# Optimization experiments

Measured on AMD Instinct MI355X. Metric: run time of the kernel, lower is better.

Reference implementation:

```python
import jax, jax.numpy as jnp
import numpy as np
import math

B, S, D, H = 2, 2048, 1024, 16
DK = D // H  # 64
THETA = 500000.0


def setup_inputs() -> dict:
    key = jax.random.key(0)
    ks = jax.random.split(key, 6)
    x = jax.random.normal(ks[0], (B, S, D), dtype=jnp.float32)
    # RoPE frequencies: inv_freq = theta^{-(2i/dk)}, angles = pos * inv_freq
    inv_freq = 1.0 / (THETA ** (jnp.arange(0, DK, 2, dtype=jnp.float32) / DK))  # [DK/2]
    angles = jnp.arange(S, dtype=jnp.float32)[:, None] * inv_freq[None, :]      # [S, DK/2]
    freqs_cos = jnp.cos(angles)
    freqs_sin = jnp.sin(angles)
    # causal additive mask [B, S, S]: 0 on/below diagonal, -1e9 above
    causal = jnp.tril(jnp.ones((S, S), dtype=bool))
    mask = jnp.where(causal, 0.0, -1e9).astype(jnp.float32)
    mask = jnp.broadcast_to(mask, (B, S, S))
    scale = 0.02
    wq = jax.random.normal(ks[1], (D, D), dtype=jnp.float32) * scale
    wk = jax.random.normal(ks[2], (D, D), dtype=jnp.float32) * scale
    wv = jax.random.normal(ks[3], (D, D), dtype=jnp.float32) * scale
    wo = jax.random.normal(ks[4], (D, D), dtype=jnp.float32) * scale
    return {"x": x, "freqs_cos": freqs_cos, "freqs_sin": freqs_sin,
            "mask": mask, "wq": wq, "wk": wk, "wv": wv, "wo": wo}


def _apply_rope(t, cos, sin):
    # t: [B, S, H, DK]; cos/sin: [S, DK/2]
    tr = t.reshape(*t.shape[:-1], DK // 2, 2)
    t0, t1 = tr[..., 0], tr[..., 1]
    c = cos[None, :, None, :]
    s = sin[None, :, None, :]
    out = jnp.stack([t0 * c - t1 * s, t0 * s + t1 * c], axis=-1)
    return out.reshape(*t.shape)


def reference(x, freqs_cos, freqs_sin, mask, wq, wk, wv, wo):
    b, s, d = x.shape
    # nn.Linear(bias=False): y = x @ W^T, W is [out, in]
    q = jnp.einsum('bsd,ed->bse', x, wq).reshape(b, s, H, DK)
    k = jnp.einsum('bsd,ed->bse', x, wk).reshape(b, s, H, DK)
    v = jnp.einsum('bsd,ed->bse', x, wv).reshape(b, s, H, DK)
    q = _apply_rope(q, freqs_cos, freqs_sin)
    k = _apply_rope(k, freqs_cos, freqs_sin)
    inv_sqrt_dk = 1.0 / math.sqrt(DK)
    # scores: [B, H, S, S]
    scores = jnp.einsum('bqhd,bkhd->bhqk', q, k) * inv_sqrt_dk
    scores = scores + mask[:, None, :, :]
    # NOTE: the original module divides by sqrt(d_k) a SECOND time before softmax
    attn = jax.nn.softmax(scores * inv_sqrt_dk, axis=-1)
    out = jnp.einsum('bhqk,bkhd->bqhd', attn, v).reshape(b, s, d)
    return jnp.einsum('bsd,ed->bse', out, wo)
```

## Files before the change

kernel.cpp:

```cpp
#include <hip/hip_runtime.h>
#include <stdint.h>

#define Bq 2
#define Sq 2048
#define Dq 1024
#define Hq 16
#define DKq 64

typedef unsigned short u16;
typedef __attribute__((ext_vector_type(8))) __bf16 bf8;
typedef __attribute__((ext_vector_type(4))) __bf16 bf4;
typedef __attribute__((ext_vector_type(4))) float fx4;
typedef __attribute__((ext_vector_type(8))) unsigned short us8;
typedef __attribute__((ext_vector_type(4))) unsigned short us4;

__device__ __forceinline__ u16 f2bf(float f) {
    union { float f; unsigned int i; } v; v.f = f;
    unsigned int r = v.i + 0x7FFFu + ((v.i >> 16) & 1u);
    return (u16)(r >> 16);
}

__device__ __forceinline__ void gll16(const void* g, void* l) {
    typedef __attribute__((address_space(1))) void GV;
    typedef __attribute__((address_space(3))) void LV;
    __builtin_amdgcn_global_load_lds((GV*)g, (LV*)l, 16, 0, 0);
}

__global__ void __launch_bounds__(256) cvt_all(const float* __restrict__ x,
                                               const float* __restrict__ wq,
                                               const float* __restrict__ wk,
                                               const float* __restrict__ wv,
                                               const float* __restrict__ wo,
                                               u16* __restrict__ ws) {
    int blk = blockIdx.x;
    const float* s;
    u16* d;
    int i;
    if (blk < 4096)      { s = x;  d = ws;           i = blk * 256 + threadIdx.x; }
    else if (blk < 5120) { s = wq; d = ws + 4194304; i = (blk - 4096) * 256 + threadIdx.x; }
    else if (blk < 6144) { s = wk; d = ws + 5242880; i = (blk - 5120) * 256 + threadIdx.x; }
    else if (blk < 7168) { s = wv; d = ws + 6291456; i = (blk - 6144) * 256 + threadIdx.x; }
    else                 { s = wo; d = ws + 7340032; i = (blk - 7168) * 256 + threadIdx.x; }
    float4 v = *(const float4*)(s + (size_t)i * 4);
    us4 o;
    o[0] = f2bf(v.x); o[1] = f2bf(v.y); o[2] = f2bf(v.z); o[3] = f2bf(v.w);
    *(us4*)(d + (size_t)i * 4) = o;
}

template<int MODE>
__global__ void __launch_bounds__(256) gemm_bt(
    const u16* __restrict__ A,
    const u16* __restrict__ W0, const u16* __restrict__ W1, const u16* __restrict__ W2,
    u16* __restrict__ O0, u16* __restrict__ O1, u16* __restrict__ O2,
    float* __restrict__ Of,
    const float* __restrict__ fc, const float* __restrict__ fs)
{
    constexpr int K = 1024;
    __shared__ __align__(16) u16 As[2][128 * 32];
    __shared__ __align__(16) u16 Bs[2][128 * 32];
    const int tid = threadIdx.x;
    const int lane = tid & 63, wid = tid >> 6;
    const int wr = wid >> 1, wc = wid & 1;
    const int fr = lane & 15, fq = lane >> 4;

    int L = blockIdx.x + 8 * (blockIdx.y + 32 * blockIdx.z);
    int chunk = gridDim.z * 4;
    int X = L & 7, C = L >> 3;
    int bx = C & 7;
    int P = X * chunk + (C >> 3);
    int by = P & 31, bz = P >> 5;
    const int m0 = by * 128, n0 = bx * 128;

    const u16* Wm = W0;
    u16* Ob = O0;
    if (MODE == 1) {
        if (bz == 1)      { Wm = W1; Ob = O1; }
        else if (bz == 2) { Wm = W2; Ob = O2; }
    }

    const int arow = tid >> 2;
    const int acol = (tid & 3) * 8;
    const u16* ga = A  + (size_t)(m0 + arow) * K + acol;
    const u16* gb = Wm + (size_t)(n0 + arow) * K + acol;

    fx4 acc[4][4] = {};

    gll16(ga,          As[0] + tid * 8);
    gll16(ga + 64 * K, As[0] + tid * 8 + 2048);
    gll16(gb,          Bs[0] + tid * 8);
    gll16(gb + 64 * K, Bs[0] + tid * 8 + 2048);
    __syncthreads();
    int cur = 0;

    for (int k0 = 0; k0 < K; k0 += 32) {
        if (k0 + 32 < K) {
            const u16* gan = ga + k0 + 32;
            const u16* gbn = gb + k0 + 32;
            gll16(gan,          As[cur ^ 1] + tid * 8);
            gll16(gan + 64 * K, As[cur ^ 1] + tid * 8 + 2048);
            gll16(gbn,          Bs[cur ^ 1] + tid * 8);
            gll16(gbn + 64 * K, Bs[cur ^ 1] + tid * 8 + 2048);
        }
        bf8 af[4], bfv[4];
        #pragma unroll
        for (int i = 0; i < 4; ++i)
            af[i] = *(const bf8*)(&As[cur][(wr * 64 + i * 16 + fr) * 32 + fq * 8]);
        #pragma unroll
        for (int j = 0; j < 4; ++j)
            bfv[j] = *(const bf8*)(&Bs[cur][(wc * 64 + j * 16 + fr) * 32 + fq * 8]);
        #pragma unroll
        for (int i = 0; i < 4; ++i)
            #pragma unroll
            for (int j = 0; j < 4; ++j)
                acc[i][j] = __builtin_amdgcn_mfma_f32_16x16x32_bf16(af[i], bfv[j], acc[i][j], 0, 0, 0);
        __syncthreads();
        cur ^= 1;
    }

    if (MODE == 0) {
        #pragma unroll
        for (int i = 0; i < 4; ++i)
            #pragma unroll
            for (int j = 0; j < 4; ++j)
                #pragma unroll
                for (int r = 0; r < 4; ++r) {
                    int m = m0 + wr * 64 + i * 16 + fq * 4 + r;
                    int n = n0 + wc * 64 + j * 16 + fr;
                    Of[(size_t)m * 1024 + n] = acc[i][j][r];
                }
    } else if (bz == 2) {
        #pragma unroll
        for (int i = 0; i < 4; ++i)
            #pragma unroll
            for (int j = 0; j < 4; ++j) {
                int n = n0 + wc * 64 + j * 16 + fr;
                int mb = m0 + wr * 64 + i * 16 + fq * 4;
                int b = mb >> 11, s = mb & 2047;
                int h = n >> 6, dk = n & 63;
                bf4 pk;
                #pragma unroll
                for (int r = 0; r < 4; ++r) pk[r] = (__bf16)acc[i][j][r];
                *(bf4*)((__bf16*)Ob + (((size_t)(b * Hq + h)) * DKq + dk) * Sq + s) = pk;
            }
    } else {
        #pragma unroll
        for (int i = 0; i < 4; ++i)
            #pragma unroll
            for (int j = 0; j < 4; ++j) {
                int n = n0 + wc * 64 + j * 16 + fr;
                int h = n >> 6, dk = n & 63;
                int ip = dk >> 1;
                float sgn = (dk & 1) ? 1.f : -1.f;
                #pragma unroll
                for (int r = 0; r < 4; ++r) {
                    int m = m0 + wr * 64 + i * 16 + fq * 4 + r;
                    int b = m >> 11, s = m & 2047;
                    float v = acc[i][j][r];
                    float pv = __shfl_xor(v, 1);
                    float c  = fc[s * 32 + ip];
                    float sn = fs[s * 32 + ip];
                    float o = v * c + sgn * pv * sn;
                    ((__bf16*)Ob)[(((size_t)(b * Hq + h)) * Sq + s) * DKq + dk] = (__bf16)o;
                }
            }
    }
}

__device__ __forceinline__ int swz(int row) { return ((row & 7) ^ ((row >> 3) & 7)) << 4; }

__global__ void __launch_bounds__(512, 4) attn_k(const u16* __restrict__ Q,
                                                 const u16* __restrict__ Kg,
                                                 const u16* __restrict__ Vtg,
                                                 u16* __restrict__ AO) {
    int L = blockIdx.x + 32 * blockIdx.y;
    int X = L & 7, C = L >> 3;
    const int bh = X * 4 + (C & 3);
    const int Qt = 31 - (C >> 2);
    const int b = bh >> 4, h = bh & 15;
    const int tid = threadIdx.x, lane = tid & 63, wid = tid >> 6;
    const int wq4 = wid & 3, par = wid >> 2;
    const int fr = lane & 15, fq = lane >> 4;
    const int swzfr = swz(fr);

    __shared__ __align__(16) u16 Ks[2][64 * 64];
    __shared__ __align__(16) u16 Vs[2][64 * 64];
    __shared__ __align__(16) u16 Ps[8][16 * 64];
    __shared__ float Lx[4][64];

    const u16* Kp = Kg  + (size_t)bh * Sq * 64;
    const u16* Vp = Vtg + (size_t)bh * 64 * Sq;
    const int q0 = Qt * 64;
    const int nt = Qt + 1;
    const int NS = (nt + 1) >> 1;

    bf8 qf0, qf1;
    {
        const u16* Qp = Q + ((size_t)bh * Sq + q0) * 64;
        int qr = wq4 * 16 + fr;
        qf0 = *(const bf8*)(Qp + qr * 64 + fq * 8);
        qf1 = *(const bf8*)(Qp + qr * 64 + fq * 8 + 32);
    }

    fx4 oacc[4] = {};
    float l_loc = 0.f;

    const int srow = tid >> 3;
    const int sce  = (tid & 7) * 8;
    const int ldst = srow * 128 + (((tid & 7) * 16) ^ swz(srow));

    us8 kreg[2], vreg[2];
    #pragma unroll
    for (int c = 0; c < 2; ++c) {
        int t = c < nt ? c : nt - 1;
        kreg[c] = *(const us8*)(Kp + ((size_t)t * 64 + srow) * 64 + sce);
        vreg[c] = *(const us8*)(Vp + (size_t)srow * Sq + t * 64 + sce);
    }
    #pragma unroll
    for (int c = 0; c < 2; ++c) {
        *(us8*)((char*)Ks[c] + ldst) = kreg[c];
        *(us8*)((char*)Vs[c] + ldst) = vreg[c];
    }
    if (NS > 1) {
        #pragma unroll
        for (int c = 0; c < 2; ++c) {
            int t = 2 + c < nt ? 2 + c : nt - 1;
            kreg[c] = *(const us8*)(Kp + ((size_t)t * 64 + srow) * 64 + sce);
            vreg[c] = *(const us8*)(Vp + (size_t)srow * Sq + t * 64 + sce);
        }
    }
    __syncthreads();

    #pragma unroll 1
    for (int sp = 0; sp < NS; ++sp) {
        const int t = 2 * sp + par;
        if (t < nt) {
            const char* Kb = (const char*)Ks[par];
            const char* Vb = (const char*)Vs[par];
            char* Pw = (char*)Ps[wid] + fr * 128;

            fx4 sf[4];
            __builtin_amdgcn_s_setprio(1);
            #pragma unroll
            for (int sj = 0; sj < 4; ++sj) {
                int krow = sj * 16 + fr;
                bf8 kf0 = *(const bf8*)(Kb + krow * 128 + ((fq * 16) ^ swz(krow)));
                bf8 kf1 = *(const bf8*)(Kb + krow * 128 + ((64 + fq * 16) ^ swz(krow)));
                fx4 a = {0.f, 0.f, 0.f, 0.f};
                a = __builtin_amdgcn_mfma_f32_16x16x32_bf16(kf0, qf0, a, 0, 0, 0);
                a = __builtin_amdgcn_mfma_f32_16x16x32_bf16(kf1, qf1, a, 0, 0, 0);
                sf[sj] = a;
            }
            __builtin_amdgcn_s_setprio(0);

            float pv[4][4];
            #pragma unroll
            for (int sj = 0; sj < 4; ++sj)
                #pragma unroll
                for (int r = 0; r < 4; ++r)
                    pv[sj][r] = __expf(sf[sj][r] * 0.015625f);
            if (t == Qt) {
                int ql = wq4 * 16 + fr;
                #pragma unroll
                for (int sj = 0; sj < 4; ++sj)
                    #pragma unroll
                    for (int r = 0; r < 4; ++r)
                        if (sj * 16 + fq * 4 + r > ql) pv[sj][r] = 0.f;
            }
            #pragma unroll
            for (int sj = 0; sj < 4; ++sj) {
                bf4 w;
                #pragma unroll
                for (int r = 0; r < 4; ++r) { w[r] = (__bf16)pv[sj][r]; l_loc += pv[sj][r]; }
                *(bf4*)(Pw + ((sj * 32 + fq * 8) ^ swzfr)) = w;
            }

            __builtin_amdgcn_s_setprio(1);
            #pragma unroll
            for (int kk = 0; kk < 2; ++kk) {
                bf8 pf = *(const bf8*)(Pw + ((kk * 64 + fq * 16) ^ swzfr));
                #pragma unroll
                for (int mf = 0; mf < 4; ++mf) {
                    int vrow = mf * 16 + fr;
                    bf8 vf = *(const bf8*)(Vb + vrow * 128 + ((kk * 64 + fq * 16) ^ swz(vrow)));
                    oacc[mf] = __builtin_amdgcn_mfma_f32_16x16x32_bf16(vf, pf, oacc[mf], 0, 0, 0);
                }
            }
            __builtin_amdgcn_s_setprio(0);
        }
        __syncthreads();
        if (sp + 1 < NS) {
            #pragma unroll
            for (int c = 0; c < 2; ++c) {
                *(us8*)((char*)Ks[c] + ldst) = kreg[c];
                *(us8*)((char*)Vs[c] + ldst) = vreg[c];
            }
            if (sp + 2 < NS) {
                #pragma unroll
                for (int c = 0; c < 2; ++c) {
                    int tt = 2 * (sp + 2) + c; if (tt > nt - 1) tt = nt - 1;
                    kreg[c] = *(const us8*)(Kp + ((size_t)tt * 64 + srow) * 64 + sce);
                    vreg[c] = *(const us8*)(Vp + (size_t)srow * Sq + tt * 64 + sce);
                }
            }
            __syncthreads();
        }
    }

    l_loc += __shfl_xor(l_loc, 16);
    l_loc += __shfl_xor(l_loc, 32);
    if (par == 1) {
        float* ob = (float*)Ps + wq4 * 1024;
        #pragma unroll
        for (int mf = 0; mf < 4; ++mf)
            *(fx4*)(ob + lane * 16 + mf * 4) = oacc[mf];
        Lx[wq4][lane] = l_loc;
    }
    __syncthreads();
    if (par == 0) {
        const float* ob = (float*)Ps + wq4 * 1024;
        float lt = l_loc + Lx[wq4][lane];
        float linv = __builtin_amdgcn_rcpf(lt);
        int s = q0 + wq4 * 16 + fr;
        #pragma unroll
        for (int mf = 0; mf < 4; ++mf) {
            fx4 oh = *(const fx4*)(ob + lane * 16 + mf * 4);
            bf4 pk;
            #pragma unroll
            for (int r = 0; r < 4; ++r) pk[r] = (__bf16)((oacc[mf][r] + oh[r]) * linv);
            *(bf4*)((__bf16*)AO + ((size_t)(b * Sq + s)) * Dq + h * 64 + mf * 16 + fq * 4) = pk;
        }
    }
}

extern "C" void kernel_launch(void* const* d_in, const int* in_sizes, int n_in,
                              void* d_out, int out_size, void* d_ws, size_t ws_size,
                              hipStream_t stream) {
    const float* x  = (const float*)d_in[0];
    const float* fc = (const float*)d_in[1];
    const float* fs = (const float*)d_in[2];
    const float* wq = (const float*)d_in[4];
    const float* wk = (const float*)d_in[5];
    const float* wv = (const float*)d_in[6];
    const float* wo = (const float*)d_in[7];
    float* out = (float*)d_out;

    u16* ws  = (u16*)d_ws;
    u16* xb  = ws;
    u16* wqb = ws + 4194304;
    u16* wkb = ws + 5242880;
    u16* wvb = ws + 6291456;
    u16* wob = ws + 7340032;
    u16* Qb  = ws + 8388608;
    u16* Kb  = ws + 12582912;
    u16* Vb  = ws + 16777216;
    u16* AOb = ws + 20971520;

    cvt_all<<<8192, 256, 0, stream>>>(x, wq, wk, wv, wo, ws);

    dim3 g1(8, 32, 3);
    gemm_bt<1><<<g1, 256, 0, stream>>>(xb, wqb, wkb, wvb, Qb, Kb, Vb, nullptr, fc, fs);

    dim3 g2(32, 32, 1);
    attn_k<<<g2, 512, 0, stream>>>(Qb, Kb, Vb, AOb);

    dim3 g3(8, 32, 1);
    gemm_bt<0><<<g3, 256, 0, stream>>>(AOb, wob, nullptr, nullptr, nullptr, nullptr, nullptr, out, nullptr, nullptr);
}
```

Measured before the change: 124.1 us.

## Triple-buffer GEMM LDS tiles with explicit vmcnt waits and split barriers

```diff
diff --git a/kernel.cpp b/kernel.cpp
--- a/kernel.cpp
+++ b/kernel.cpp
@@ -24,6 +24,10 @@
     typedef __attribute__((address_space(1))) void GV;
     typedef __attribute__((address_space(3))) void LV;
     __builtin_amdgcn_global_load_lds((GV*)g, (LV*)l, 16, 0, 0);
+}
+
+template<int N> __device__ __forceinline__ void waitv() {
+    asm volatile("s_waitcnt vmcnt(%0)" :: "n"(N) : "memory");
 }
 
 __global__ void __launch_bounds__(256) cvt_all(const float* __restrict__ x,
@@ -56,8 +60,9 @@
     const float* __restrict__ fc, const float* __restrict__ fs)
 {
     constexpr int K = 1024;
-    __shared__ __align__(16) u16 As[2][128 * 32];
-    __shared__ __align__(16) u16 Bs[2][128 * 32];
+    constexpr int NT = K / 32;
+    __shared__ __align__(16) u16 As[3][128 * 32];
+    __shared__ __align__(16) u16 Bs[3][128 * 32];
     const int tid = threadIdx.x;
     const int lane = tid & 63, wid = tid >> 6;
     const int wr = wid >> 1, wc = wid & 1;
@@ -85,37 +90,56 @@
 
     fx4 acc[4][4] = {};
 
-    gll16(ga,          As[0] + tid * 8);
-    gll16(ga + 64 * K, As[0] + tid * 8 + 2048);
-    gll16(gb,          Bs[0] + tid * 8);
-    gll16(gb + 64 * K, Bs[0] + tid * 8 + 2048);
-    __syncthreads();
-    int cur = 0;
-
-    for (int k0 = 0; k0 < K; k0 += 32) {
-        if (k0 + 32 < K) {
-            const u16* gan = ga + k0 + 32;
-            const u16* gbn = gb + k0 + 32;
-            gll16(gan,          As[cur ^ 1] + tid * 8);
-            gll16(gan + 64 * K, As[cur ^ 1] + tid * 8 + 2048);
-            gll16(gbn,          Bs[cur ^ 1] + tid * 8);
-            gll16(gbn + 64 * K, Bs[cur ^ 1] + tid * 8 + 2048);
-        }
+    auto STAGE = [&](int t, int bufi) {
+        const u16* gan = ga + t * 32;
+        const u16* gbn = gb + t * 32;
+        gll16(gan,          As[bufi] + tid * 8);
+        gll16(gan + 64 * K, As[bufi] + tid * 8 + 2048);
+        gll16(gbn,          Bs[bufi] + tid * 8);
+        gll16(gbn + 64 * K, Bs[bufi] + tid * 8 + 2048);
+    };
+    auto COMPUTE = [&](int bufi) {
         bf8 af[4], bfv[4];
         #pragma unroll
         for (int i = 0; i < 4; ++i)
-            af[i] = *(const bf8*)(&As[cur][(wr * 64 + i * 16 + fr) * 32 + fq * 8]);
+            af[i] = *(const bf8*)(&As[bufi][(wr * 64 + i * 16 + fr) * 32 + fq * 8]);
         #pragma unroll
         for (int j = 0; j < 4; ++j)
-            bfv[j] = *(const bf8*)(&Bs[cur][(wc * 64 + j * 16 + fr) * 32 + fq * 8]);
+            bfv[j] = *(const bf8*)(&Bs[bufi][(wc * 64 + j * 16 + fr) * 32 + fq * 8]);
         #pragma unroll
         for (int i = 0; i < 4; ++i)
             #pragma unroll
             for (int j = 0; j < 4; ++j)
                 acc[i][j] = __builtin_amdgcn_mfma_f32_16x16x32_bf16(af[i], bfv[j], acc[i][j], 0, 0, 0);
-        __syncthreads();
-        cur ^= 1;
-    }
+    };
+
+    STAGE(0, 0); STAGE(1, 1); STAGE(2, 2);
+
+    int cur = 0;
+    #pragma unroll 1
+    for (int t = 0; t < NT - 2; ++t) {
+        waitv<8>();
+        __builtin_amdgcn_sched_barrier(0);
+        __builtin_amdgcn_s_barrier();
+        __builtin_amdgcn_sched_barrier(0);
+        COMPUTE(cur);
+        __builtin_amdgcn_sched_barrier(0);
+        __builtin_amdgcn_s_barrier();
+        __builtin_amdgcn_sched_barrier(0);
+        if (t < NT - 3) STAGE(t + 3, cur);
+        cur = cur == 2 ? 0 : cur + 1;
+    }
+    waitv<4>();
+    __builtin_amdgcn_sched_barrier(0);
+    __builtin_amdgcn_s_barrier();
+    __builtin_amdgcn_sched_barrier(0);
+    COMPUTE(cur);
+    cur = cur == 2 ? 0 : cur + 1;
+    waitv<0>();
+    __builtin_amdgcn_sched_barrier(0);
+    __builtin_amdgcn_s_barrier();
+    __builtin_amdgcn_sched_barrier(0);
+    COMPUTE(cur);
 
     if (MODE == 0) {
         #pragma unroll
```

Measured after the change: 121.8 us. Within noise of the previous version (-1.9%).
